# Performance work log

Hardware: AMD Instinct MI355X
Metric: run time of the kernel (lower is better)

## Reference

```python
import jax, jax.numpy as jnp
import numpy as np

N = 10000
E = 160000
DIMS = [256, 256, 256, 256]
EPS = 1e-5
DSCALE = 1.0
SPE_IDX = 0


def setup_inputs() -> dict:
    key = jax.random.key(0)
    ks = jax.random.split(key, 40)
    inp = {}
    inp['x'] = jax.random.normal(ks[0], (N, DIMS[0]), dtype=jnp.float32)
    inp['src'] = jax.random.randint(ks[1], (E,), 0, N, dtype=jnp.int32)
    inp['dst'] = jax.random.randint(ks[2], (E,), 0, N, dtype=jnp.int32)
    k = 3
    for i, (din, dout) in enumerate(zip(DIMS[:-1], DIMS[1:])):
        s = 1.0 / np.sqrt(din)
        inp[f'Ws{i}'] = jax.random.uniform(ks[k], (din, dout), jnp.float32, -s, s); k += 1
        inp[f'Wn{i}'] = jax.random.uniform(ks[k], (din, dout), jnp.float32, -s, s); k += 1
        inp[f'b{i}'] = jnp.zeros((dout,), jnp.float32)
        inp[f'g{i}'] = jnp.ones((dout,), jnp.float32)
        inp[f'be{i}'] = jnp.zeros((dout,), jnp.float32)
    return inp


def _sage(h, src, dst, Ws, Wn, b):
    # mean aggregation over in-neighbors: segment-sum gathered src feats over dst
    agg = jax.ops.segment_sum(h[src], dst, num_segments=N)          # [N, din]
    deg = jax.ops.segment_sum(jnp.ones((E,), h.dtype), dst, num_segments=N)
    mean = agg / jnp.maximum(deg, 1.0)[:, None]
    return h @ Ws + mean @ Wn + b


def _bn(h, g, be):
    # BatchNorm1d, training mode (biased batch variance)
    mu = jnp.mean(h, axis=0)
    var = jnp.mean((h - mu) ** 2, axis=0)
    return (h - mu) * jax.lax.rsqrt(var + EPS) * g + be


def reference(x, src, dst, Ws0, Wn0, b0, g0, be0, Ws1, Wn1, b1, g1, be1,
              Ws2, Wn2, b2, g2, be2):
    params = [(Ws0, Wn0, b0, g0, be0), (Ws1, Wn1, b1, g1, be1),
              (Ws2, Wn2, b2, g2, be2)]
    n_layers = len(params)
    outs = x
    for i, (Ws, Wn, b, g, be) in enumerate(params):
        outs = _sage(outs, src, dst, Ws, Wn, b)
        # hid side-outputs (sigmoid(outs*dscale)[spe_idx]) don't affect outs path
        outs = _bn(outs, g, be)
        if i != n_layers - 1:
            outs = jax.nn.relu(outs)
        else:
            outs = jax.nn.sigmoid(outs)
    return outs
```

## Files before the change

### kernel.cpp

```cpp
#include <hip/hip_runtime.h>
#include <math.h>

#define NN 10000
#define EE 160000
#define DIM 256
#define KK 512
#define CAP 64
#define EPS_BN 1e-5f
#define AST 516

typedef __attribute__((ext_vector_type(8)))  short bf16x8;
typedef __attribute__((ext_vector_type(16))) float f32x16;

union U16 { uint2 u2[2]; bf16x8 v; };

static __device__ __forceinline__ unsigned short f2bf(float f) {
    unsigned u = __float_as_uint(f);
    unsigned r = (u + 0x7fffu + ((u >> 16) & 1u)) >> 16;
    return (unsigned short)r;
}
static __device__ __forceinline__ float bflo(unsigned v) { return __uint_as_float(v << 16); }
static __device__ __forceinline__ float bfhi(unsigned v) { return __uint_as_float(v & 0xffff0000u); }
static __device__ __forceinline__ unsigned packbf(float a, float b) {
    return (unsigned)f2bf(a) | ((unsigned)f2bf(b) << 16);
}

struct Params {
    const float* x; const int* src; const int* dst;
    const float *Ws0, *Wn0, *Ws1, *Wn1, *Ws2, *Wn2;
    const float *g0, *be0, *g1, *be1, *g2, *be2;
    float* out;
    unsigned short* hx;
    unsigned short* z0;
    unsigned short* z1;
    unsigned short* wcat;
    float* stats;
    int* cnt;
    int* slots;
};

static __device__ __forceinline__ void accum8(float* a, uint4 v) {
    a[0] += bflo(v.x); a[1] += bfhi(v.x);
    a[2] += bflo(v.y); a[3] += bfhi(v.y);
    a[4] += bflo(v.z); a[5] += bfhi(v.z);
    a[6] += bflo(v.w); a[7] += bfhi(v.w);
}
static __device__ __forceinline__ void accum8n(float* a, uint4 v,
                                               const float* sc, const float* sh) {
    a[0] += fmaxf(bflo(v.x) * sc[0] + sh[0], 0.f);
    a[1] += fmaxf(bfhi(v.x) * sc[1] + sh[1], 0.f);
    a[2] += fmaxf(bflo(v.y) * sc[2] + sh[2], 0.f);
    a[3] += fmaxf(bfhi(v.y) * sc[3] + sh[3], 0.f);
    a[4] += fmaxf(bflo(v.z) * sc[4] + sh[4], 0.f);
    a[5] += fmaxf(bfhi(v.z) * sc[5] + sh[5], 0.f);
    a[6] += fmaxf(bflo(v.w) * sc[6] + sh[6], 0.f);
    a[7] += fmaxf(bfhi(v.w) * sc[7] + sh[7], 0.f);
}

__global__ __launch_bounds__(256) void k_prep(Params P) {
    int g0 = blockIdx.x * 256 + threadIdx.x;
    int stride = gridDim.x * 256;
    for (int g = g0; g < NN * 64; g += stride) {
        int r = g >> 6, c4 = (g & 63) * 4;
        float4 v = *(const float4*)(P.x + (size_t)r * DIM + c4);
        uint2 p; p.x = packbf(v.x, v.y); p.y = packbf(v.z, v.w);
        *(uint2*)(P.hx + (size_t)r * DIM + c4) = p;
    }
    for (int g = g0; g < 3 * DIM * KK; g += stride) {
        int L = g >> 17; int i = g & 131071;
        int k = i >> 8, n = i & 255;
        const float* Ws = (L == 0) ? P.Ws0 : ((L == 1) ? P.Ws1 : P.Ws2);
        const float* Wn = (L == 0) ? P.Wn0 : ((L == 1) ? P.Wn1 : P.Wn2);
        float v = (k < DIM) ? Ws[(size_t)k * DIM + n] : Wn[(size_t)(k - DIM) * DIM + n];
        P.wcat[(size_t)L * DIM * KK + (size_t)n * KK + k] = f2bf(v);
    }
    for (int g = g0; g < NN + 6 * DIM; g += stride) {
        if (g < NN) P.cnt[g] = 0;
        else P.stats[g - NN] = 0.f;
    }
}

__global__ __launch_bounds__(256) void k_bucket(Params P) {
    int e = blockIdx.x * 256 + threadIdx.x;
    if (e < EE) {
        int d = P.dst[e];
        int p = atomicAdd(&P.cnt[d], 1);
        if (p < CAP) P.slots[(size_t)d * CAP + p] = P.src[e];
    }
}

__global__ __launch_bounds__(512, 2) void k_ag(Params P, int L,
                                               const unsigned short* __restrict__ gsrc,
                                               unsigned short* __restrict__ gdst) {
    __shared__ unsigned short At[32][AST];
    int t = threadIdx.x;
    int wave = t >> 6, lane = t & 63;
    int h = lane >> 5, l = lane & 31;

    float sc[8], sh[8];
    if (L > 0) {
        const float* st = P.stats + (L - 1) * 2 * DIM;
        const float* gam = (L == 1) ? P.g0 : P.g1;
        const float* bet = (L == 1) ? P.be0 : P.be1;
#pragma unroll
        for (int i = 0; i < 8; ++i) {
            int c = l * 8 + i;
            float mu  = st[c] * (1.0f / NN);
            float var = st[DIM + c] * (1.0f / NN) - mu * mu;
            float k = rsqrtf(var + EPS_BN) * gam[c];
            sc[i] = k;
            sh[i] = bet[c] - mu * k;
        }
    }
    const uint4* srcm = (const uint4*)gsrc;

    int node0 = blockIdx.x * 32 + wave * 4;
    int4 c4 = *(const int4*)(P.cnt + node0);
    int cs[4] = {c4.x, c4.y, c4.z, c4.w};
    int slv[4];
    uint4 own[4];
#pragma unroll
    for (int i = 0; i < 4; ++i) {
        int node = node0 + i;
        int nc = (node < NN) ? node : (NN - 1);
        slv[i] = P.slots[(size_t)nc * CAP + lane];
        own[i] = srcm[(size_t)nc * 32 + l];
    }
#pragma unroll
    for (int i = 0; i < 4; ++i) {
        int m = wave * 4 + i;
        int node = node0 + i;
        unsigned short* arow = &At[m][0];
        if (node >= NN) {
            if (h == 0) {
                uint2 z2 = make_uint2(0u, 0u);
                *(uint2*)(arow + l * 8)           = z2;
                *(uint2*)(arow + l * 8 + 4)       = z2;
                *(uint2*)(arow + 256 + l * 8)     = z2;
                *(uint2*)(arow + 256 + l * 8 + 4) = z2;
            }
            continue;
        }
        int cnt = cs[i]; if (cnt > CAP) cnt = CAP;
        int sv = slv[i];
        if (h == 0) {
            uint4 z = own[i];
            uint4 o;
            if (L > 0) {
                o.x = packbf(fmaxf(bflo(z.x) * sc[0] + sh[0], 0.f),
                             fmaxf(bfhi(z.x) * sc[1] + sh[1], 0.f));
                o.y = packbf(fmaxf(bflo(z.y) * sc[2] + sh[2], 0.f),
                             fmaxf(bfhi(z.y) * sc[3] + sh[3], 0.f));
                o.z = packbf(fmaxf(bflo(z.z) * sc[4] + sh[4], 0.f),
                             fmaxf(bfhi(z.z) * sc[5] + sh[5], 0.f));
                o.w = packbf(fmaxf(bflo(z.w) * sc[6] + sh[6], 0.f),
                             fmaxf(bfhi(z.w) * sc[7] + sh[7], 0.f));
            } else o = z;
            *(uint2*)(arow + l * 8)     = make_uint2(o.x, o.y);
            *(uint2*)(arow + l * 8 + 4) = make_uint2(o.z, o.w);
        }
        float a[8] = {0, 0, 0, 0, 0, 0, 0, 0};
        int j = 0;
        for (; j + 15 < cnt; j += 16) {
            int r0 = __shfl(sv, j +  0 + h), r1 = __shfl(sv, j +  2 + h);
            int r2 = __shfl(sv, j +  4 + h), r3 = __shfl(sv, j +  6 + h);
            int r4 = __shfl(sv, j +  8 + h), r5 = __shfl(sv, j + 10 + h);
            int r6 = __shfl(sv, j + 12 + h), r7 = __shfl(sv, j + 14 + h);
            uint4 v0 = srcm[(size_t)r0 * 32 + l];
            uint4 v1 = srcm[(size_t)r1 * 32 + l];
            uint4 v2 = srcm[(size_t)r2 * 32 + l];
            uint4 v3 = srcm[(size_t)r3 * 32 + l];
            uint4 v4 = srcm[(size_t)r4 * 32 + l];
            uint4 v5 = srcm[(size_t)r5 * 32 + l];
            uint4 v6 = srcm[(size_t)r6 * 32 + l];
            uint4 v7 = srcm[(size_t)r7 * 32 + l];
            if (L == 0) {
                accum8(a, v0); accum8(a, v1); accum8(a, v2); accum8(a, v3);
                accum8(a, v4); accum8(a, v5); accum8(a, v6); accum8(a, v7);
            } else {
                accum8n(a, v0, sc, sh); accum8n(a, v1, sc, sh);
                accum8n(a, v2, sc, sh); accum8n(a, v3, sc, sh);
                accum8n(a, v4, sc, sh); accum8n(a, v5, sc, sh);
                accum8n(a, v6, sc, sh); accum8n(a, v7, sc, sh);
            }
        }
        for (; j + 3 < cnt; j += 4) {
            int r0 = __shfl(sv, j + h), r1 = __shfl(sv, j + 2 + h);
            uint4 v0 = srcm[(size_t)r0 * 32 + l];
            uint4 v1 = srcm[(size_t)r1 * 32 + l];
            if (L == 0) { accum8(a, v0); accum8(a, v1); }
            else { accum8n(a, v0, sc, sh); accum8n(a, v1, sc, sh); }
        }
        for (; j + 1 < cnt; j += 2) {
            int r0 = __shfl(sv, j + h);
            uint4 v0 = srcm[(size_t)r0 * 32 + l];
            if (L == 0) accum8(a, v0); else accum8n(a, v0, sc, sh);
        }
        if (j < cnt) {
            int r0 = __shfl(sv, cnt - 1);
            uint4 v0 = srcm[(size_t)r0 * 32 + l];
            if (h == 0) {
                if (L == 0) accum8(a, v0); else accum8n(a, v0, sc, sh);
            }
        }
#pragma unroll
        for (int q = 0; q < 8; ++q) a[q] += __shfl_xor(a[q], 32);
        if (h == 0) {
            float inv = 1.0f / (float)(cnt > 1 ? cnt : 1);
            *(uint2*)(arow + 256 + l * 8)     = make_uint2(packbf(a[0] * inv, a[1] * inv),
                                                           packbf(a[2] * inv, a[3] * inv));
            *(uint2*)(arow + 256 + l * 8 + 4) = make_uint2(packbf(a[4] * inv, a[5] * inv),
                                                           packbf(a[6] * inv, a[7] * inv));
        }
    }
    __syncthreads();

    const unsigned short* wcatL = P.wcat + (size_t)L * DIM * KK;
    float* statsL = P.stats + L * 2 * DIM;
    int m = l;
    int row0 = blockIdx.x * 32;
    int colw0 = wave * 32;
    const unsigned short* Bp = wcatL + (size_t)(colw0 + m) * KK + h * 8;
    const unsigned short* Arow = &At[m][0];
    f32x16 acc;
#pragma unroll
    for (int i = 0; i < 16; ++i) acc[i] = 0.f;
#pragma unroll 8
    for (int k0 = 0; k0 < KK; k0 += 16) {
        U16 ua;
        ua.u2[0] = *(const uint2*)(Arow + k0 + h * 8);
        ua.u2[1] = *(const uint2*)(Arow + k0 + h * 8 + 4);
        bf16x8 av = ua.v;
        bf16x8 bv = *(const bf16x8*)(Bp + k0);
        acc = __builtin_amdgcn_mfma_f32_32x32x16_bf16(av, bv, acc, 0, 0, 0);
    }
    int cc = colw0 + m;
    float s = 0.f, s2 = 0.f;
#pragma unroll
    for (int reg = 0; reg < 16; ++reg) {
        int r = row0 + (reg & 3) + 8 * (reg >> 2) + 4 * h;
        if (r < NN) {
            float v = acc[reg];
            gdst[(size_t)r * DIM + cc] = f2bf(v);
            s += v; s2 += v * v;
        }
    }
    s  += __shfl_down(s, 32);
    s2 += __shfl_down(s2, 32);
    if (h == 0) {
        atomicAdd(&statsL[cc], s);
        atomicAdd(&statsL[DIM + cc], s2);
    }
}

__global__ __launch_bounds__(256) void k_norm(Params P) {
    const float* statsL = P.stats + 2 * 2 * DIM;
    int t = threadIdx.x;
    int c8 = (t & 31) * 8;
    int r = blockIdx.x * 8 + (t >> 5);
    float sc[8], sh[8];
#pragma unroll
    for (int i = 0; i < 8; ++i) {
        int c = c8 + i;
        float mu  = statsL[c] * (1.0f / NN);
        float var = statsL[DIM + c] * (1.0f / NN) - mu * mu;
        float k = rsqrtf(var + EPS_BN) * P.g2[c];
        sc[i] = k;
        sh[i] = P.be2[c] - mu * k;
    }
    uint4 v = *(const uint4*)(P.z0 + (size_t)r * DIM + c8);
    float f[8] = {bflo(v.x), bfhi(v.x), bflo(v.y), bfhi(v.y),
                  bflo(v.z), bfhi(v.z), bflo(v.w), bfhi(v.w)};
#pragma unroll
    for (int i = 0; i < 8; ++i) f[i] = f[i] * sc[i] + sh[i];
    float4 o0, o1;
    o0.x = 1.0f / (1.0f + __expf(-f[0]));
    o0.y = 1.0f / (1.0f + __expf(-f[1]));
    o0.z = 1.0f / (1.0f + __expf(-f[2]));
    o0.w = 1.0f / (1.0f + __expf(-f[3]));
    o1.x = 1.0f / (1.0f + __expf(-f[4]));
    o1.y = 1.0f / (1.0f + __expf(-f[5]));
    o1.z = 1.0f / (1.0f + __expf(-f[6]));
    o1.w = 1.0f / (1.0f + __expf(-f[7]));
    *(float4*)(P.out + (size_t)r * DIM + c8)     = o0;
    *(float4*)(P.out + (size_t)r * DIM + c8 + 4) = o1;
}

extern "C" void kernel_launch(void* const* d_in, const int* in_sizes, int n_in,
                              void* d_out, int out_size, void* d_ws, size_t ws_size,
                              hipStream_t stream) {
    Params P;
    P.x   = (const float*)d_in[0];
    P.src = (const int*)d_in[1];
    P.dst = (const int*)d_in[2];
    P.Ws0 = (const float*)d_in[3];  P.Wn0 = (const float*)d_in[4];
    P.g0  = (const float*)d_in[6];  P.be0 = (const float*)d_in[7];
    P.Ws1 = (const float*)d_in[8];  P.Wn1 = (const float*)d_in[9];
    P.g1  = (const float*)d_in[11]; P.be1 = (const float*)d_in[12];
    P.Ws2 = (const float*)d_in[13]; P.Wn2 = (const float*)d_in[14];
    P.g2  = (const float*)d_in[16]; P.be2 = (const float*)d_in[17];
    P.out = (float*)d_out;

    char* ws = (char*)d_ws;
    size_t off = 0;
    P.hx   = (unsigned short*)(ws + off); off += (size_t)NN * DIM * 2;
    P.z0   = (unsigned short*)(ws + off); off += (size_t)NN * DIM * 2;
    P.z1   = (unsigned short*)(ws + off); off += (size_t)NN * DIM * 2;
    P.wcat = (unsigned short*)(ws + off); off += (size_t)3 * DIM * KK * 2;
    P.stats = (float*)(ws + off); off += 3 * 2 * DIM * sizeof(float);
    P.cnt   = (int*)(ws + off); off += (size_t)NN * 4; off = (off + 255) & ~(size_t)255;
    P.slots = (int*)(ws + off); off += (size_t)NN * CAP * 4;
    (void)ws_size;

    k_prep<<<512, 256, 0, stream>>>(P);
    k_bucket<<<(EE + 255) / 256, 256, 0, stream>>>(P);
    k_ag<<<313, 512, 0, stream>>>(P, 0, P.hx, P.z0);
    k_ag<<<313, 512, 0, stream>>>(P, 1, P.z0, P.z1);
    k_ag<<<313, 512, 0, stream>>>(P, 2, P.z1, P.z0);
    k_norm<<<NN / 8, 256, 0, stream>>>(P);
}
```

Baseline: 249.7 us.

## Split fused gather+GEMM into separate normalize, gather and GEMM kernels

Splits the fused aggregate-and-GEMM kernel into three kernels. A pre-pass applies BatchNorm+ReLU once per node into a bf16 buffer. A gather kernel uses one wave per node and gives high occupancy for the irregular neighbor reads. The GEMM kernel only loads the self and mean rows into shared memory. This stops the scale/shift/relu from being recomputed on every gathered neighbor and separates the latency-bound gather from the compute-bound GEMM, at the cost of more launches and extra global round trips for the normalized and aggregated buffers.

```diff
diff --git a/kernel.cpp b/kernel.cpp
--- a/kernel.cpp
+++ b/kernel.cpp
@@ -33,6 +33,8 @@
     unsigned short* hx;
     unsigned short* z0;
     unsigned short* z1;
+    unsigned short* hn;
+    unsigned short* magg;
     unsigned short* wcat;
     float* stats;
     int* cnt;
@@ -44,17 +46,6 @@
     a[2] += bflo(v.y); a[3] += bfhi(v.y);
     a[4] += bflo(v.z); a[5] += bfhi(v.z);
     a[6] += bflo(v.w); a[7] += bfhi(v.w);
-}
-static __device__ __forceinline__ void accum8n(float* a, uint4 v,
-                                               const float* sc, const float* sh) {
-    a[0] += fmaxf(bflo(v.x) * sc[0] + sh[0], 0.f);
-    a[1] += fmaxf(bfhi(v.x) * sc[1] + sh[1], 0.f);
-    a[2] += fmaxf(bflo(v.y) * sc[2] + sh[2], 0.f);
-    a[3] += fmaxf(bfhi(v.y) * sc[3] + sh[3], 0.f);
-    a[4] += fmaxf(bflo(v.z) * sc[4] + sh[4], 0.f);
-    a[5] += fmaxf(bfhi(v.z) * sc[5] + sh[5], 0.f);
-    a[6] += fmaxf(bflo(v.w) * sc[6] + sh[6], 0.f);
-    a[7] += fmaxf(bfhi(v.w) * sc[7] + sh[7], 0.f);
 }
 
 __global__ __launch_bounds__(256) void k_prep(Params P) {
@@ -89,128 +80,126 @@
     }
 }
 
-__global__ __launch_bounds__(512, 2) void k_ag(Params P, int L,
-                                               const unsigned short* __restrict__ gsrc,
-                                               unsigned short* __restrict__ gdst) {
+__global__ __launch_bounds__(256) void k_pre(Params P, int Lprev,
+                                             const unsigned short* __restrict__ z,
+                                             unsigned short* __restrict__ hn) {
+    const float* st  = P.stats + Lprev * 2 * DIM;
+    const float* gam = (Lprev == 0) ? P.g0 : P.g1;
+    const float* bet = (Lprev == 0) ? P.be0 : P.be1;
+    int t = threadIdx.x;
+    int c8 = (t & 31) * 8;
+    int r = blockIdx.x * 8 + (t >> 5);
+    float sc[8], sh[8];
+#pragma unroll
+    for (int i = 0; i < 8; ++i) {
+        int c = c8 + i;
+        float mu  = st[c] * (1.0f / NN);
+        float var = st[DIM + c] * (1.0f / NN) - mu * mu;
+        float k = rsqrtf(var + EPS_BN) * gam[c];
+        sc[i] = k;
+        sh[i] = bet[c] - mu * k;
+    }
+    uint4 v = *(const uint4*)(z + (size_t)r * DIM + c8);
+    uint4 o;
+    o.x = packbf(fmaxf(bflo(v.x) * sc[0] + sh[0], 0.f),
+                 fmaxf(bfhi(v.x) * sc[1] + sh[1], 0.f));
+    o.y = packbf(fmaxf(bflo(v.y) * sc[2] + sh[2], 0.f),
+                 fmaxf(bfhi(v.y) * sc[3] + sh[3], 0.f));
+    o.z = packbf(fmaxf(bflo(v.z) * sc[4] + sh[4], 0.f),
+                 fmaxf(bfhi(v.z) * sc[5] + sh[5], 0.f));
+    o.w = packbf(fmaxf(bflo(v.w) * sc[6] + sh[6], 0.f),
+                 fmaxf(bfhi(v.w) * sc[7] + sh[7], 0.f));
+    *(uint4*)(hn + (size_t)r * DIM + c8) = o;
+}
+
+__global__ __launch_bounds__(256) void k_gather(Params P,
+                                                const unsigned short* __restrict__ hsrc,
+                                                unsigned short* __restrict__ magg) {
+    int t = threadIdx.x;
+    int wave = t >> 6, lane = t & 63;
+    int h = lane >> 5, l = lane & 31;
+    int node = blockIdx.x * 4 + wave;
+    if (node >= NN) return;
+    int cnt = P.cnt[node]; if (cnt > CAP) cnt = CAP;
+    int sv = P.slots[(size_t)node * CAP + lane];
+    const uint4* srcm = (const uint4*)hsrc;
+    float a[8] = {0, 0, 0, 0, 0, 0, 0, 0};
+    int j = 0;
+    for (; j + 15 < cnt; j += 16) {
+        int r0 = __shfl(sv, j +  0 + h), r1 = __shfl(sv, j +  2 + h);
+        int r2 = __shfl(sv, j +  4 + h), r3 = __shfl(sv, j +  6 + h);
+        int r4 = __shfl(sv, j +  8 + h), r5 = __shfl(sv, j + 10 + h);
+        int r6 = __shfl(sv, j + 12 + h), r7 = __shfl(sv, j + 14 + h);
+        uint4 v0 = srcm[(size_t)r0 * 32 + l];
+        uint4 v1 = srcm[(size_t)r1 * 32 + l];
+        uint4 v2 = srcm[(size_t)r2 * 32 + l];
+        uint4 v3 = srcm[(size_t)r3 * 32 + l];
+        uint4 v4 = srcm[(size_t)r4 * 32 + l];
+        uint4 v5 = srcm[(size_t)r5 * 32 + l];
+        uint4 v6 = srcm[(size_t)r6 * 32 + l];
+        uint4 v7 = srcm[(size_t)r7 * 32 + l];
+        accum8(a, v0); accum8(a, v1); accum8(a, v2); accum8(a, v3);
+        accum8(a, v4); accum8(a, v5); accum8(a, v6); accum8(a, v7);
+    }
+    for (; j + 3 < cnt; j += 4) {
+        int r0 = __shfl(sv, j + h), r1 = __shfl(sv, j + 2 + h);
+        uint4 v0 = srcm[(size_t)r0 * 32 + l];
+        uint4 v1 = srcm[(size_t)r1 * 32 + l];
+        accum8(a, v0); accum8(a, v1);
+    }
+    for (; j + 1 < cnt; j += 2) {
+        int r0 = __shfl(sv, j + h);
+        uint4 v0 = srcm[(size_t)r0 * 32 + l];
+        accum8(a, v0);
+    }
+    if (j < cnt) {
+        int r0 = __shfl(sv, cnt - 1);
+        uint4 v0 = srcm[(size_t)r0 * 32 + l];
+        if (h == 0) accum8(a, v0);
+    }
+#pragma unroll
+    for (int q = 0; q < 8; ++q) a[q] += __shfl_xor(a[q], 32);
+    if (h == 0) {
+        float inv = 1.0f / (float)(cnt > 1 ? cnt : 1);
+        uint4 o;
+        o.x = packbf(a[0] * inv, a[1] * inv);
+        o.y = packbf(a[2] * inv, a[3] * inv);
+        o.z = packbf(a[4] * inv, a[5] * inv);
+        o.w = packbf(a[6] * inv, a[7] * inv);
+        ((uint4*)magg)[(size_t)node * 32 + l] = o;
+    }
+}
+
+__global__ __launch_bounds__(512) void k_gemm(Params P, int L,
+                                              const unsigned short* __restrict__ hsrc,
+                                              const unsigned short* __restrict__ magg,
+                                              unsigned short* __restrict__ gdst) {
     __shared__ unsigned short At[32][AST];
     int t = threadIdx.x;
     int wave = t >> 6, lane = t & 63;
     int h = lane >> 5, l = lane & 31;
 
-    float sc[8], sh[8];
-    if (L > 0) {
-        const float* st = P.stats + (L - 1) * 2 * DIM;
-        const float* gam = (L == 1) ? P.g0 : P.g1;
-        const float* bet = (L == 1) ? P.be0 : P.be1;
-#pragma unroll
-        for (int i = 0; i < 8; ++i) {
-            int c = l * 8 + i;
-            float mu  = st[c] * (1.0f / NN);
-            float var = st[DIM + c] * (1.0f / NN) - mu * mu;
-            float k = rsqrtf(var + EPS_BN) * gam[c];
-            sc[i] = k;
-            sh[i] = bet[c] - mu * k;
-        }
-    }
-    const uint4* srcm = (const uint4*)gsrc;
-
-    int node0 = blockIdx.x * 32 + wave * 4;
-    int4 c4 = *(const int4*)(P.cnt + node0);
-    int cs[4] = {c4.x, c4.y, c4.z, c4.w};
-    int slv[4];
-    uint4 own[4];
-#pragma unroll
-    for (int i = 0; i < 4; ++i) {
-        int node = node0 + i;
-        int nc = (node < NN) ? node : (NN - 1);
-        slv[i] = P.slots[(size_t)nc * CAP + lane];
-        own[i] = srcm[(size_t)nc * 32 + l];
-    }
-#pragma unroll
-    for (int i = 0; i < 4; ++i) {
-        int m = wave * 4 + i;
-        int node = node0 + i;
-        unsigned short* arow = &At[m][0];
-        if (node >= NN) {
-            if (h == 0) {
-                uint2 z2 = make_uint2(0u, 0u);
-                *(uint2*)(arow + l * 8)           = z2;
-                *(uint2*)(arow + l * 8 + 4)       = z2;
-                *(uint2*)(arow + 256 + l * 8)     = z2;
-                *(uint2*)(arow + 256 + l * 8 + 4) = z2;
-            }
-            continue;
-        }
-        int cnt = cs[i]; if (cnt > CAP) cnt = CAP;
-        int sv = slv[i];
-        if (h == 0) {
-            uint4 z = own[i];
-            uint4 o;
-            if (L > 0) {
-                o.x = packbf(fmaxf(bflo(z.x) * sc[0] + sh[0], 0.f),
-                             fmaxf(bfhi(z.x) * sc[1] + sh[1], 0.f));
-                o.y = packbf(fmaxf(bflo(z.y) * sc[2] + sh[2], 0.f),
-                             fmaxf(bfhi(z.y) * sc[3] + sh[3], 0.f));
-                o.z = packbf(fmaxf(bflo(z.z) * sc[4] + sh[4], 0.f),
-                             fmaxf(bfhi(z.z) * sc[5] + sh[5], 0.f));
-                o.w = packbf(fmaxf(bflo(z.w) * sc[6] + sh[6], 0.f),
-                             fmaxf(bfhi(z.w) * sc[7] + sh[7], 0.f));
-            } else o = z;
-            *(uint2*)(arow + l * 8)     = make_uint2(o.x, o.y);
-            *(uint2*)(arow + l * 8 + 4) = make_uint2(o.z, o.w);
-        }
-        float a[8] = {0, 0, 0, 0, 0, 0, 0, 0};
-        int j = 0;
-        for (; j + 15 < cnt; j += 16) {
-            int r0 = __shfl(sv, j +  0 + h), r1 = __shfl(sv, j +  2 + h);
-            int r2 = __shfl(sv, j +  4 + h), r3 = __shfl(sv, j +  6 + h);
-            int r4 = __shfl(sv, j +  8 + h), r5 = __shfl(sv, j + 10 + h);
-            int r6 = __shfl(sv, j + 12 + h), r7 = __shfl(sv, j + 14 + h);
-            uint4 v0 = srcm[(size_t)r0 * 32 + l];
-            uint4 v1 = srcm[(size_t)r1 * 32 + l];
-            uint4 v2 = srcm[(size_t)r2 * 32 + l];
-            uint4 v3 = srcm[(size_t)r3 * 32 + l];
-            uint4 v4 = srcm[(size_t)r4 * 32 + l];
-            uint4 v5 = srcm[(size_t)r5 * 32 + l];
-            uint4 v6 = srcm[(size_t)r6 * 32 + l];
-            uint4 v7 = srcm[(size_t)r7 * 32 + l];
-            if (L == 0) {
-                accum8(a, v0); accum8(a, v1); accum8(a, v2); accum8(a, v3);
-                accum8(a, v4); accum8(a, v5); accum8(a, v6); accum8(a, v7);
-            } else {
-                accum8n(a, v0, sc, sh); accum8n(a, v1, sc, sh);
-                accum8n(a, v2, sc, sh); accum8n(a, v3, sc, sh);
-                accum8n(a, v4, sc, sh); accum8n(a, v5, sc, sh);
-                accum8n(a, v6, sc, sh); accum8n(a, v7, sc, sh);
-            }
-        }
-        for (; j + 3 < cnt; j += 4) {
-            int r0 = __shfl(sv, j + h), r1 = __shfl(sv, j + 2 + h);
-            uint4 v0 = srcm[(size_t)r0 * 32 + l];
-            uint4 v1 = srcm[(size_t)r1 * 32 + l];
-            if (L == 0) { accum8(a, v0); accum8(a, v1); }
-            else { accum8n(a, v0, sc, sh); accum8n(a, v1, sc, sh); }
-        }
-        for (; j + 1 < cnt; j += 2) {
-            int r0 = __shfl(sv, j + h);
-            uint4 v0 = srcm[(size_t)r0 * 32 + l];
-            if (L == 0) accum8(a, v0); else accum8n(a, v0, sc, sh);
-        }
-        if (j < cnt) {
-            int r0 = __shfl(sv, cnt - 1);
-            uint4 v0 = srcm[(size_t)r0 * 32 + l];
-            if (h == 0) {
-                if (L == 0) accum8(a, v0); else accum8n(a, v0, sc, sh);
-            }
-        }
-#pragma unroll
-        for (int q = 0; q < 8; ++q) a[q] += __shfl_xor(a[q], 32);
-        if (h == 0) {
-            float inv = 1.0f / (float)(cnt > 1 ? cnt : 1);
-            *(uint2*)(arow + 256 + l * 8)     = make_uint2(packbf(a[0] * inv, a[1] * inv),
-                                                           packbf(a[2] * inv, a[3] * inv));
-            *(uint2*)(arow + 256 + l * 8 + 4) = make_uint2(packbf(a[4] * inv, a[5] * inv),
-                                                           packbf(a[6] * inv, a[7] * inv));
+    {
+        int r = t >> 4, q = t & 15;
+        int node = blockIdx.x * 32 + r;
+        const unsigned short* srcp = (q < 8) ? hsrc : magg;
+        int c0 = (q & 7) * 32;
+        unsigned short* dstp = &At[r][(q < 8 ? 0 : 256) + c0];
+        if (node < NN) {
+            const uint4* gp = (const uint4*)(srcp + (size_t)node * DIM + c0);
+            uint4 v0 = gp[0], v1 = gp[1], v2 = gp[2], v3 = gp[3];
+            *(uint2*)(dstp)      = make_uint2(v0.x, v0.y);
+            *(uint2*)(dstp + 4)  = make_uint2(v0.z, v0.w);
+            *(uint2*)(dstp + 8)  = make_uint2(v1.x, v1.y);
+            *(uint2*)(dstp + 12) = make_uint2(v1.z, v1.w);
+            *(uint2*)(dstp + 16) = make_uint2(v2.x, v2.y);
+            *(uint2*)(dstp + 20) = make_uint2(v2.z, v2.w);
+            *(uint2*)(dstp + 24) = make_uint2(v3.x, v3.y);
+            *(uint2*)(dstp + 28) = make_uint2(v3.z, v3.w);
+        } else {
+            uint2 z = make_uint2(0u, 0u);
+#pragma unroll
+            for (int q8 = 0; q8 < 8; ++q8) *(uint2*)(dstp + q8 * 4) = z;
         }
     }
     __syncthreads();
@@ -306,6 +295,8 @@
     P.hx   = (unsigned short*)(ws + off); off += (size_t)NN * DIM * 2;
     P.z0   = (unsigned short*)(ws + off); off += (size_t)NN * DIM * 2;
     P.z1   = (unsigned short*)(ws + off); off += (size_t)NN * DIM * 2;
+    P.hn   = (unsigned short*)(ws + off); off += (size_t)NN * DIM * 2;
+    P.magg = (unsigned short*)(ws + off); off += (size_t)NN * DIM * 2;
     P.wcat = (unsigned short*)(ws + off); off += (size_t)3 * DIM * KK * 2;
     P.stats = (float*)(ws + off); off += 3 * 2 * DIM * sizeof(float);
     P.cnt   = (int*)(ws + off); off += (size_t)NN * 4; off = (off + 255) & ~(size_t)255;
@@ -314,8 +305,13 @@
 
     k_prep<<<512, 256, 0, stream>>>(P);
     k_bucket<<<(EE + 255) / 256, 256, 0, stream>>>(P);
-    k_ag<<<313, 512, 0, stream>>>(P, 0, P.hx, P.z0);
-    k_ag<<<313, 512, 0, stream>>>(P, 1, P.z0, P.z1);
-    k_ag<<<313, 512, 0, stream>>>(P, 2, P.z1, P.z0);
+    k_gather<<<2500, 256, 0, stream>>>(P, P.hx, P.magg);
+    k_gemm<<<313, 512, 0, stream>>>(P, 0, P.hx, P.magg, P.z0);
+    k_pre<<<1250, 256, 0, stream>>>(P, 0, P.z0, P.hn);
+    k_gather<<<2500, 256, 0, stream>>>(P, P.hn, P.magg);
+    k_gemm<<<313, 512, 0, stream>>>(P, 1, P.hn, P.magg, P.z1);
+    k_pre<<<1250, 256, 0, stream>>>(P, 1, P.z1, P.hn);
+    k_gather<<<2500, 256, 0, stream>>>(P, P.hn, P.magg);
+    k_gemm<<<313, 512, 0, stream>>>(P, 2, P.hn, P.magg, P.z0);
     k_norm<<<NN / 8, 256, 0, stream>>>(P);
 }
```

Result: faster. 220.0 us (-11.9%).

## Split fused gather+GEMM kernel into separate gather and GEMM kernels

Applied to the files above, without the earlier changes.

The fused aggregate-and-matmul kernel is split in two. A fine-grained gather kernel uses one wave per node across 2500 blocks and writes the mean-aggregated features to a new bf16 buffer. A GEMM kernel then loads the self and aggregated rows into shared memory and runs the MFMA matmul. This is meant to raise parallelism and latency hiding for the irregular gather, which previously ran on only 313 blocks. In exchange it adds a global round-trip of the aggregated features, three extra kernel launches, and a redundant BN-scale computation in the gather kernel.

```diff
diff --git a/kernel.cpp b/kernel.cpp
--- a/kernel.cpp
+++ b/kernel.cpp
@@ -33,6 +33,7 @@
     unsigned short* hx;
     unsigned short* z0;
     unsigned short* z1;
+    unsigned short* magg;
     unsigned short* wcat;
     float* stats;
     int* cnt;
@@ -89,17 +90,16 @@
     }
 }
 
-__global__ __launch_bounds__(512, 2) void k_ag(Params P, int L,
-                                               const unsigned short* __restrict__ gsrc,
-                                               unsigned short* __restrict__ gdst) {
-    __shared__ unsigned short At[32][AST];
+__global__ __launch_bounds__(256) void k_gather(Params P, int L,
+                                                const unsigned short* __restrict__ hsrc,
+                                                unsigned short* __restrict__ magg) {
     int t = threadIdx.x;
     int wave = t >> 6, lane = t & 63;
     int h = lane >> 5, l = lane & 31;
 
     float sc[8], sh[8];
     if (L > 0) {
-        const float* st = P.stats + (L - 1) * 2 * DIM;
+        const float* st  = P.stats + (L - 1) * 2 * DIM;
         const float* gam = (L == 1) ? P.g0 : P.g1;
         const float* bet = (L == 1) ? P.be0 : P.be1;
 #pragma unroll
@@ -112,105 +112,125 @@
             sh[i] = bet[c] - mu * k;
         }
     }
-    const uint4* srcm = (const uint4*)gsrc;
-
-    int node0 = blockIdx.x * 32 + wave * 4;
-    int4 c4 = *(const int4*)(P.cnt + node0);
-    int cs[4] = {c4.x, c4.y, c4.z, c4.w};
-    int slv[4];
-    uint4 own[4];
-#pragma unroll
-    for (int i = 0; i < 4; ++i) {
-        int node = node0 + i;
-        int nc = (node < NN) ? node : (NN - 1);
-        slv[i] = P.slots[(size_t)nc * CAP + lane];
-        own[i] = srcm[(size_t)nc * 32 + l];
-    }
-#pragma unroll
-    for (int i = 0; i < 4; ++i) {
-        int m = wave * 4 + i;
-        int node = node0 + i;
-        unsigned short* arow = &At[m][0];
-        if (node >= NN) {
-            if (h == 0) {
+    int node = blockIdx.x * 4 + wave;
+    if (node >= NN) return;
+    int cnt = P.cnt[node]; if (cnt > CAP) cnt = CAP;
+    int sv = P.slots[(size_t)node * CAP + lane];
+    const uint4* srcm = (const uint4*)hsrc;
+    float a[8] = {0, 0, 0, 0, 0, 0, 0, 0};
+    int j = 0;
+    for (; j + 15 < cnt; j += 16) {
+        int r0 = __shfl(sv, j +  0 + h), r1 = __shfl(sv, j +  2 + h);
+        int r2 = __shfl(sv, j +  4 + h), r3 = __shfl(sv, j +  6 + h);
+        int r4 = __shfl(sv, j +  8 + h), r5 = __shfl(sv, j + 10 + h);
+        int r6 = __shfl(sv, j + 12 + h), r7 = __shfl(sv, j + 14 + h);
+        uint4 v0 = srcm[(size_t)r0 * 32 + l];
+        uint4 v1 = srcm[(size_t)r1 * 32 + l];
+        uint4 v2 = srcm[(size_t)r2 * 32 + l];
+        uint4 v3 = srcm[(size_t)r3 * 32 + l];
+        uint4 v4 = srcm[(size_t)r4 * 32 + l];
+        uint4 v5 = srcm[(size_t)r5 * 32 + l];
+        uint4 v6 = srcm[(size_t)r6 * 32 + l];
+        uint4 v7 = srcm[(size_t)r7 * 32 + l];
+        if (L == 0) {
+            accum8(a, v0); accum8(a, v1); accum8(a, v2); accum8(a, v3);
+            accum8(a, v4); accum8(a, v5); accum8(a, v6); accum8(a, v7);
+        } else {
+            accum8n(a, v0, sc, sh); accum8n(a, v1, sc, sh);
+            accum8n(a, v2, sc, sh); accum8n(a, v3, sc, sh);
+            accum8n(a, v4, sc, sh); accum8n(a, v5, sc, sh);
+            accum8n(a, v6, sc, sh); accum8n(a, v7, sc, sh);
+        }
+    }
+    for (; j + 3 < cnt; j += 4) {
+        int r0 = __shfl(sv, j + h), r1 = __shfl(sv, j + 2 + h);
+        uint4 v0 = srcm[(size_t)r0 * 32 + l];
+        uint4 v1 = srcm[(size_t)r1 * 32 + l];
+        if (L == 0) { accum8(a, v0); accum8(a, v1); }
+        else { accum8n(a, v0, sc, sh); accum8n(a, v1, sc, sh); }
+    }
+    for (; j + 1 < cnt; j += 2) {
+        int r0 = __shfl(sv, j + h);
+        uint4 v0 = srcm[(size_t)r0 * 32 + l];
+        if (L == 0) accum8(a, v0); else accum8n(a, v0, sc, sh);
+    }
+    if (j < cnt) {
+        int r0 = __shfl(sv, cnt - 1);
+        uint4 v0 = srcm[(size_t)r0 * 32 + l];
+        if (h == 0) {
+            if (L == 0) accum8(a, v0); else accum8n(a, v0, sc, sh);
+        }
+    }
+#pragma unroll
+    for (int q = 0; q < 8; ++q) a[q] += __shfl_xor(a[q], 32);
+    if (h == 0) {
+        float inv = 1.0f / (float)(cnt > 1 ? cnt : 1);
+        uint4 o;
+        o.x = packbf(a[0] * inv, a[1] * inv);
+        o.y = packbf(a[2] * inv, a[3] * inv);
+        o.z = packbf(a[4] * inv, a[5] * inv);
+        o.w = packbf(a[6] * inv, a[7] * inv);
+        ((uint4*)magg)[(size_t)node * 32 + l] = o;
+    }
+}
+
+__global__ __launch_bounds__(512) void k_gemm(Params P, int L,
+                                              const unsigned short* __restrict__ hsrc,
+                                              const unsigned short* __restrict__ magg,
+                                              unsigned short* __restrict__ gdst) {
+    __shared__ unsigned short At[32][AST];
+    int t = threadIdx.x;
+    int wave = t >> 6, lane = t & 63;
+    int h = lane >> 5, l = lane & 31;
+
+    {
+        int cgS = t & 31, rs = t >> 5;
+        float scg[8], shg[8];
+        if (L > 0) {
+            const float* stp = P.stats + (L - 1) * 2 * DIM;
+            const float* gam = (L == 1) ? P.g0 : P.g1;
+            const float* bet = (L == 1) ? P.be0 : P.be1;
+#pragma unroll
+            for (int i = 0; i < 8; ++i) {
+                int c = cgS * 8 + i;
+                float mu  = stp[c] * (1.0f / NN);
+                float var = stp[DIM + c] * (1.0f / NN) - mu * mu;
+                float k = rsqrtf(var + EPS_BN) * gam[c];
+                scg[i] = k;
+                shg[i] = bet[c] - mu * k;
+            }
+        }
+#pragma unroll
+        for (int rr = 0; rr < 2; ++rr) {
+            int r = rs + rr * 16;
+            int node = blockIdx.x * 32 + r;
+            unsigned short* arow = &At[r][0];
+            if (node < NN) {
+                uint4 ov = *(const uint4*)(hsrc + (size_t)node * DIM + cgS * 8);
+                if (L > 0) {
+                    uint4 o;
+                    o.x = packbf(fmaxf(bflo(ov.x) * scg[0] + shg[0], 0.f),
+                                 fmaxf(bfhi(ov.x) * scg[1] + shg[1], 0.f));
+                    o.y = packbf(fmaxf(bflo(ov.y) * scg[2] + shg[2], 0.f),
+                                 fmaxf(bfhi(ov.y) * scg[3] + shg[3], 0.f));
+                    o.z = packbf(fmaxf(bflo(ov.z) * scg[4] + shg[4], 0.f),
+                                 fmaxf(bfhi(ov.z) * scg[5] + shg[5], 0.f));
+                    o.w = packbf(fmaxf(bflo(ov.w) * scg[6] + shg[6], 0.f),
+                                 fmaxf(bfhi(ov.w) * scg[7] + shg[7], 0.f));
+                    ov = o;
+                }
+                *(uint2*)(arow + cgS * 8)     = make_uint2(ov.x, ov.y);
+                *(uint2*)(arow + cgS * 8 + 4) = make_uint2(ov.z, ov.w);
+                uint4 mv = *(const uint4*)(magg + (size_t)node * DIM + cgS * 8);
+                *(uint2*)(arow + 256 + cgS * 8)     = make_uint2(mv.x, mv.y);
+                *(uint2*)(arow + 256 + cgS * 8 + 4) = make_uint2(mv.z, mv.w);
+            } else {
                 uint2 z2 = make_uint2(0u, 0u);
-                *(uint2*)(arow + l * 8)           = z2;
-                *(uint2*)(arow + l * 8 + 4)       = z2;
-                *(uint2*)(arow + 256 + l * 8)     = z2;
-                *(uint2*)(arow + 256 + l * 8 + 4) = z2;
+                *(uint2*)(arow + cgS * 8)           = z2;
+                *(uint2*)(arow + cgS * 8 + 4)       = z2;
+                *(uint2*)(arow + 256 + cgS * 8)     = z2;
+                *(uint2*)(arow + 256 + cgS * 8 + 4) = z2;
             }
-            continue;
-        }
-        int cnt = cs[i]; if (cnt > CAP) cnt = CAP;
-        int sv = slv[i];
-        if (h == 0) {
-            uint4 z = own[i];
-            uint4 o;
-            if (L > 0) {
-                o.x = packbf(fmaxf(bflo(z.x) * sc[0] + sh[0], 0.f),
-                             fmaxf(bfhi(z.x) * sc[1] + sh[1], 0.f));
-                o.y = packbf(fmaxf(bflo(z.y) * sc[2] + sh[2], 0.f),
-                             fmaxf(bfhi(z.y) * sc[3] + sh[3], 0.f));
-                o.z = packbf(fmaxf(bflo(z.z) * sc[4] + sh[4], 0.f),
-                             fmaxf(bfhi(z.z) * sc[5] + sh[5], 0.f));
-                o.w = packbf(fmaxf(bflo(z.w) * sc[6] + sh[6], 0.f),
-                             fmaxf(bfhi(z.w) * sc[7] + sh[7], 0.f));
-            } else o = z;
-            *(uint2*)(arow + l * 8)     = make_uint2(o.x, o.y);
-            *(uint2*)(arow + l * 8 + 4) = make_uint2(o.z, o.w);
-        }
-        float a[8] = {0, 0, 0, 0, 0, 0, 0, 0};
-        int j = 0;
-        for (; j + 15 < cnt; j += 16) {
-            int r0 = __shfl(sv, j +  0 + h), r1 = __shfl(sv, j +  2 + h);
-            int r2 = __shfl(sv, j +  4 + h), r3 = __shfl(sv, j +  6 + h);
-            int r4 = __shfl(sv, j +  8 + h), r5 = __shfl(sv, j + 10 + h);
-            int r6 = __shfl(sv, j + 12 + h), r7 = __shfl(sv, j + 14 + h);
-            uint4 v0 = srcm[(size_t)r0 * 32 + l];
-            uint4 v1 = srcm[(size_t)r1 * 32 + l];
-            uint4 v2 = srcm[(size_t)r2 * 32 + l];
-            uint4 v3 = srcm[(size_t)r3 * 32 + l];
-            uint4 v4 = srcm[(size_t)r4 * 32 + l];
-            uint4 v5 = srcm[(size_t)r5 * 32 + l];
-            uint4 v6 = srcm[(size_t)r6 * 32 + l];
-            uint4 v7 = srcm[(size_t)r7 * 32 + l];
-            if (L == 0) {
-                accum8(a, v0); accum8(a, v1); accum8(a, v2); accum8(a, v3);
-                accum8(a, v4); accum8(a, v5); accum8(a, v6); accum8(a, v7);
-            } else {
-                accum8n(a, v0, sc, sh); accum8n(a, v1, sc, sh);
-                accum8n(a, v2, sc, sh); accum8n(a, v3, sc, sh);
-                accum8n(a, v4, sc, sh); accum8n(a, v5, sc, sh);
-                accum8n(a, v6, sc, sh); accum8n(a, v7, sc, sh);
-            }
-        }
-        for (; j + 3 < cnt; j += 4) {
-            int r0 = __shfl(sv, j + h), r1 = __shfl(sv, j + 2 + h);
-            uint4 v0 = srcm[(size_t)r0 * 32 + l];
-            uint4 v1 = srcm[(size_t)r1 * 32 + l];
-            if (L == 0) { accum8(a, v0); accum8(a, v1); }
-            else { accum8n(a, v0, sc, sh); accum8n(a, v1, sc, sh); }
-        }
-        for (; j + 1 < cnt; j += 2) {
-            int r0 = __shfl(sv, j + h);
-            uint4 v0 = srcm[(size_t)r0 * 32 + l];
-            if (L == 0) accum8(a, v0); else accum8n(a, v0, sc, sh);
-        }
-        if (j < cnt) {
-            int r0 = __shfl(sv, cnt - 1);
-            uint4 v0 = srcm[(size_t)r0 * 32 + l];
-            if (h == 0) {
-                if (L == 0) accum8(a, v0); else accum8n(a, v0, sc, sh);
-            }
-        }
-#pragma unroll
-        for (int q = 0; q < 8; ++q) a[q] += __shfl_xor(a[q], 32);
-        if (h == 0) {
-            float inv = 1.0f / (float)(cnt > 1 ? cnt : 1);
-            *(uint2*)(arow + 256 + l * 8)     = make_uint2(packbf(a[0] * inv, a[1] * inv),
-                                                           packbf(a[2] * inv, a[3] * inv));
-            *(uint2*)(arow + 256 + l * 8 + 4) = make_uint2(packbf(a[4] * inv, a[5] * inv),
-                                                           packbf(a[6] * inv, a[7] * inv));
         }
     }
     __syncthreads();
@@ -306,6 +326,7 @@
     P.hx   = (unsigned short*)(ws + off); off += (size_t)NN * DIM * 2;
     P.z0   = (unsigned short*)(ws + off); off += (size_t)NN * DIM * 2;
     P.z1   = (unsigned short*)(ws + off); off += (size_t)NN * DIM * 2;
+    P.magg = (unsigned short*)(ws + off); off += (size_t)NN * DIM * 2;
     P.wcat = (unsigned short*)(ws + off); off += (size_t)3 * DIM * KK * 2;
     P.stats = (float*)(ws + off); off += 3 * 2 * DIM * sizeof(float);
     P.cnt   = (int*)(ws + off); off += (size_t)NN * 4; off = (off + 255) & ~(size_t)255;
@@ -314,8 +335,11 @@
 
     k_prep<<<512, 256, 0, stream>>>(P);
     k_bucket<<<(EE + 255) / 256, 256, 0, stream>>>(P);
-    k_ag<<<313, 512, 0, stream>>>(P, 0, P.hx, P.z0);
-    k_ag<<<313, 512, 0, stream>>>(P, 1, P.z0, P.z1);
-    k_ag<<<313, 512, 0, stream>>>(P, 2, P.z1, P.z0);
+    k_gather<<<2500, 256, 0, stream>>>(P, 0, P.hx, P.magg);
+    k_gemm<<<313, 512, 0, stream>>>(P, 0, P.hx, P.magg, P.z0);
+    k_gather<<<2500, 256, 0, stream>>>(P, 1, P.z0, P.magg);
+    k_gemm<<<313, 512, 0, stream>>>(P, 1, P.z0, P.magg, P.z1);
+    k_gather<<<2500, 256, 0, stream>>>(P, 2, P.z1, P.magg);
+    k_gemm<<<313, 512, 0, stream>>>(P, 2, P.z1, P.magg, P.z0);
     k_norm<<<NN / 8, 256, 0, stream>>>(P);
 }
```

Result: faster. 225.2 us (-9.8%).
